# Kernel tuning notes

Hardware: AMD Instinct MI355X
Metric: run time of the kernel (lower is better)

Reference implementation:

```python
import jax, jax.numpy as jnp
import numpy as np

B, S, D, H = 2, 2048, 1024, 16
DH = D // H  # dim_per_head = 64


def setup_inputs() -> dict:
    key = jax.random.key(0)
    ks = jax.random.split(key, 12)
    scale = 1.0 / np.sqrt(D)
    inp = {
        "key": jax.random.normal(ks[0], (B, S, D), jnp.float32),
        "value": jax.random.normal(ks[1], (B, S, D), jnp.float32),
        "query": jax.random.normal(ks[2], (B, S, D), jnp.float32),
        "mask": jax.random.randint(ks[3], (B, S, S), 0, 2) == 1,
        "Wq": jax.random.normal(ks[4], (D, D), jnp.float32) * scale,
        "bq": jnp.zeros((D,), jnp.float32),
        "Wk": jax.random.normal(ks[5], (D, D), jnp.float32) * scale,
        "bk": jnp.zeros((D,), jnp.float32),
        "Wv": jax.random.normal(ks[6], (D, D), jnp.float32) * scale,
        "bv": jnp.zeros((D,), jnp.float32),
        "Wo": jax.random.normal(ks[7], (D, D), jnp.float32) * scale,
        "bo": jnp.zeros((D,), jnp.float32),
    }
    return inp


def reference(key, value, query, mask, Wq, bq, Wk, bk, Wv, bv, Wo, bo):
    b, s, d = query.shape
    dh = d // H

    def split_heads(x):  # [b, s, d] -> [b, H, s, dh]
        return x.reshape(b, -1, H, dh).transpose(0, 2, 1, 3)

    q = split_heads(query @ Wq + bq) / jnp.sqrt(jnp.float32(dh))
    k = split_heads(key @ Wk + bk)
    v = split_heads(value @ Wv + bv)

    scores = jnp.einsum("bhqd,bhkd->bhqk", q, k)  # [b, H, s, s]
    scores = jnp.where(mask[:, None, :, :], jnp.float32(-1e18), scores)
    attn = jax.nn.softmax(scores, axis=-1)  # dropout is identity in eval
    ctx = jnp.einsum("bhqk,bhkd->bhqd", attn, v)
    ctx = ctx.transpose(0, 2, 1, 3).reshape(b, s, d)
    return ctx @ Wo + bo
```

## Files before the change

kernel.cpp:

```cpp
#include <hip/hip_runtime.h>
#include <hip/hip_bf16.h>

#define BATCH  2
#define SEQ    2048
#define DMODEL 1024
#define NHEAD  16
#define DHEAD  64
#define NTOK   (BATCH * SEQ)

using f32x4 = __attribute__((ext_vector_type(4))) float;
using s16x4 = __attribute__((ext_vector_type(4))) short;
using s16x8 = __attribute__((ext_vector_type(8))) short;

__device__ __forceinline__ short f2bf(float f) {
  __hip_bfloat16 h = __float2bfloat16(f);
  return *(short*)&h;
}

__device__ __forceinline__ void gload_lds16(const short* g, short* l) {
  __builtin_amdgcn_global_load_lds(
      (const __attribute__((address_space(1))) void*)g,
      (__attribute__((address_space(3))) void*)l, 16, 0, 0);
}

__global__ __launch_bounds__(256) void wtrans_kernel(
    const float* __restrict__ Wq, const float* __restrict__ Wk,
    const float* __restrict__ Wv, const float* __restrict__ Wo,
    short* __restrict__ Wt) {
  __shared__ short tile[64][72];
  const float* W = blockIdx.z == 0 ? Wq : blockIdx.z == 1 ? Wk
                 : blockIdx.z == 2 ? Wv : Wo;
  short* out = Wt + (size_t)blockIdx.z * DMODEL * DMODEL;
  int k0 = blockIdx.x * 64, n0 = blockIdx.y * 64;
  int t = threadIdx.x;
#pragma unroll
  for (int i = 0; i < 4; ++i) {
    int idx = t + i * 256;
    int row = idx >> 4, c4 = idx & 15;
    f32x4 v = *(const f32x4*)(W + (size_t)(k0 + row) * DMODEL + n0 + c4 * 4);
    s16x4 p;
    p[0] = f2bf(v[0]); p[1] = f2bf(v[1]); p[2] = f2bf(v[2]); p[3] = f2bf(v[3]);
    *(s16x4*)&tile[row][c4 * 4] = p;
  }
  __syncthreads();
#pragma unroll
  for (int i = 0; i < 2; ++i) {
    int idx = t + i * 256;
    int nrow = idx >> 3, c8 = idx & 7;
    s16x8 p;
#pragma unroll
    for (int j = 0; j < 8; ++j) p[j] = tile[c8 * 8 + j][nrow];
    *(s16x8*)(out + (size_t)(n0 + nrow) * DMODEL + k0 + c8 * 8) = p;
  }
}

__global__ __launch_bounds__(256) void mpack_kernel(
    const int* __restrict__ mask, unsigned long long* __restrict__ Mp) {
  const int total_words = BATCH * SEQ * (SEQ / 64);
  int lane = threadIdx.x & 63;
  int wv = blockIdx.x * 4 + (threadIdx.x >> 6);
  int nw = gridDim.x * 4;
  for (int w = wv; w < total_words; w += nw) {
    int mv = mask[(size_t)w * 64 + lane];
    unsigned long long bits = __ballot(mv != 0);
    if (lane == 0) Mp[w] = bits;
  }
}

__global__ __launch_bounds__(256) void proj_qkv_kernel(
    const float* __restrict__ Xq, const float* __restrict__ Xk,
    const float* __restrict__ Xv, const short* __restrict__ Wt,
    const float* __restrict__ bq, const float* __restrict__ bk,
    const float* __restrict__ bv, short* __restrict__ QKV) {
  __shared__ short As[128][32];
  __shared__ short Bs[128][32];
  const int sel = blockIdx.z;
  const float* X    = sel == 0 ? Xq : sel == 1 ? Xk : Xv;
  const float* bias = sel == 0 ? bq : sel == 1 ? bk : bv;
  const short* Wsel = Wt + (size_t)sel * DMODEL * DMODEL;
  short* Obuf = QKV + (size_t)sel * ((size_t)BATCH * NHEAD * SEQ * DHEAD);
  const float scale = sel == 0 ? 0.18033688011111793f : 1.0f;

  int m0 = blockIdx.x * 128, n0 = blockIdx.y * 128;
  int t = threadIdx.x, wid = t >> 6, lane = t & 63;
  int lr = lane & 15, lg = lane >> 4;
  int wr = wid >> 1, wc = wid & 1;
  f32x4 acc[4][4] = {};

  for (int kt = 0; kt < DMODEL / 32; ++kt) {
    int k0 = kt * 32;
    __syncthreads();
#pragma unroll
    for (int i = 0; i < 2; ++i) {
      int c = i * 256 + t;
      short* lbase = &Bs[0][0] + (size_t)((i * 256 + (t & ~63)) << 3);
      gload_lds16(Wsel + (size_t)(n0 + (c >> 2)) * DMODEL + k0 + ((c & 3) << 3),
                  lbase);
    }
#pragma unroll
    for (int i = 0; i < 2; ++i) {
      int idx = t + i * 256, row = idx >> 2, c8 = idx & 3;
      const float* src = X + (size_t)(m0 + row) * DMODEL + k0 + c8 * 8;
      f32x4 v0 = *(const f32x4*)src;
      f32x4 v1 = *(const f32x4*)(src + 4);
      s16x8 p;
      p[0] = f2bf(v0[0]); p[1] = f2bf(v0[1]); p[2] = f2bf(v0[2]); p[3] = f2bf(v0[3]);
      p[4] = f2bf(v1[0]); p[5] = f2bf(v1[1]); p[6] = f2bf(v1[2]); p[7] = f2bf(v1[3]);
      *(s16x8*)&As[row][c8 * 8] = p;
    }
    __syncthreads();
    s16x8 afr[4], bfr[4];
#pragma unroll
    for (int mi = 0; mi < 4; ++mi)
      afr[mi] = *(const s16x8*)&As[wr * 64 + mi * 16 + lr][lg * 8];
#pragma unroll
    for (int ni = 0; ni < 4; ++ni)
      bfr[ni] = *(const s16x8*)&Bs[wc * 64 + ni * 16 + lr][lg * 8];
#pragma unroll
    for (int mi = 0; mi < 4; ++mi)
#pragma unroll
      for (int ni = 0; ni < 4; ++ni)
        acc[mi][ni] = __builtin_amdgcn_mfma_f32_16x16x32_bf16(
            afr[mi], bfr[ni], acc[mi][ni], 0, 0, 0);
  }
#pragma unroll
  for (int mi = 0; mi < 4; ++mi)
#pragma unroll
    for (int ni = 0; ni < 4; ++ni) {
      int n = n0 + wc * 64 + ni * 16 + lr;
      float bv_ = bias[n];
      int h = n >> 6, d = n & 63;
#pragma unroll
      for (int r = 0; r < 4; ++r) {
        int m = m0 + wr * 64 + mi * 16 + lg * 4 + r;
        int b = m >> 11, s = m & (SEQ - 1);
        float val = (acc[mi][ni][r] + bv_) * scale;
        Obuf[((size_t)(b * NHEAD + h) * SEQ + s) * DHEAD + d] = f2bf(val);
      }
    }
}

__global__ __launch_bounds__(256) void attn_kernel(
    const short* __restrict__ Qb, const short* __restrict__ Kb,
    const short* __restrict__ Vb, const unsigned long long* __restrict__ Mp,
    short* __restrict__ Ctx) {
  __shared__ short Ks[64 * 64];
  __shared__ short Vt[64 * 64];
  __shared__ short Ps[4 * 16 * 64];
  int qt = blockIdx.x, bh = blockIdx.y;
  int b = bh >> 4, h = bh & 15;
  int q0 = qt * 64;
  int t = threadIdx.x, wid = t >> 6, lane = t & 63;
  int lr = lane & 15, lg = lane >> 4;
  int lr7 = lr & 7;

  const short* Qrow = Qb + ((size_t)bh * SEQ + q0 + wid * 16 + lr) * DHEAD;
  s16x8 qf[2];
  qf[0] = *(const s16x8*)(Qrow + lg * 8);
  qf[1] = *(const s16x8*)(Qrow + 32 + lg * 8);

  const short* KbBase = Kb + (size_t)bh * SEQ * DHEAD;
  const short* VbBase = Vb + (size_t)bh * SEQ * DHEAD;

  float m_run = -1e30f, l_run = 0.f;
  f32x4 o_acc[4] = {};

  const unsigned long long* mrow =
      Mp + ((size_t)b * SEQ + q0 + wid * 16 + lr) * (SEQ / 64);
  unsigned long long mw = mrow[0];

  s16x8 kreg[2], vreg[2];
#pragma unroll
  for (int i = 0; i < 2; ++i) {
    kreg[i] = *(const s16x8*)(KbBase + (size_t)((t >> 3) + i * 32) * DHEAD + (t & 7) * 8);
    vreg[i] = *(const s16x8*)(VbBase + (size_t)lane * DHEAD + (wid + i * 4) * 8);
  }

  for (int kt = 0; kt < SEQ / 64; ++kt) {
    unsigned long long mw_cur = mw;
    __syncthreads();
#pragma unroll
    for (int i = 0; i < 2; ++i) {
      int krow = (t >> 3) + i * 32, kc = t & 7;
      *(s16x8*)&Ks[krow * 64 + ((kc ^ (krow & 7)) << 3)] = kreg[i];
      int vc8 = wid + i * 4;
#pragma unroll
      for (int j = 0; j < 8; ++j) {
        int d = vc8 * 8 + j;
        Vt[d * 64 + ((((lane >> 3) ^ (d & 7)) << 3) | (lane & 7))] = vreg[i][j];
      }
    }
    __syncthreads();
    if (kt + 1 < SEQ / 64) {
      int k0n = (kt + 1) * 64;
#pragma unroll
      for (int i = 0; i < 2; ++i) {
        kreg[i] = *(const s16x8*)(KbBase + (size_t)(k0n + (t >> 3) + i * 32) * DHEAD + (t & 7) * 8);
        vreg[i] = *(const s16x8*)(VbBase + (size_t)(k0n + lane) * DHEAD + (wid + i * 4) * 8);
      }
      mw = mrow[kt + 1];
    }

    f32x4 sfr[4];
    __builtin_amdgcn_s_setprio(1);
#pragma unroll
    for (int nf = 0; nf < 4; ++nf) {
      int row = nf * 16 + lr;
      s16x8 kf0 = *(const s16x8*)&Ks[row * 64 + ((lg ^ lr7) << 3)];
      s16x8 kf1 = *(const s16x8*)&Ks[row * 64 + (((4 + lg) ^ lr7) << 3)];
      f32x4 c = {};
      c = __builtin_amdgcn_mfma_f32_16x16x32_bf16(kf0, qf[0], c, 0, 0, 0);
      c = __builtin_amdgcn_mfma_f32_16x16x32_bf16(kf1, qf[1], c, 0, 0, 0);
      sfr[nf] = c;
    }
    __builtin_amdgcn_s_setprio(0);

    unsigned w0 = (unsigned)(mw_cur >> (lg * 4));
    unsigned w1 = (unsigned)(mw_cur >> (lg * 4 + 32));
#pragma unroll
    for (int nf = 0; nf < 4; ++nf)
#pragma unroll
      for (int r = 0; r < 4; ++r) {
        unsigned bit = (nf < 2) ? (w0 >> (nf * 16 + r)) : (w1 >> ((nf - 2) * 16 + r));
        if (bit & 1u) sfr[nf][r] = -1e30f;
      }
    float tm = fmaxf(fmaxf(fmaxf(sfr[0][0], sfr[0][1]), fmaxf(sfr[0][2], sfr[0][3])),
                     fmaxf(fmaxf(sfr[1][0], sfr[1][1]), fmaxf(sfr[1][2], sfr[1][3])));
    float tm2 = fmaxf(fmaxf(fmaxf(sfr[2][0], sfr[2][1]), fmaxf(sfr[2][2], sfr[2][3])),
                      fmaxf(fmaxf(sfr[3][0], sfr[3][1]), fmaxf(sfr[3][2], sfr[3][3])));
    tm = fmaxf(tm, tm2);
    tm = fmaxf(tm, __shfl_xor(tm, 16, 64));
    tm = fmaxf(tm, __shfl_xor(tm, 32, 64));

    bool small = __all(tm <= m_run + 8.0f);
    if (!small) {
      float mnew = fmaxf(m_run, tm);
      float scl = __builtin_amdgcn_exp2f(m_run - mnew);
      m_run = mnew;
      l_run *= scl;
      float scl_o[4];
#pragma unroll
      for (int r = 0; r < 4; ++r) scl_o[r] = __shfl(scl, lg * 4 + r, 64);
#pragma unroll
      for (int nf = 0; nf < 4; ++nf)
#pragma unroll
        for (int r = 0; r < 4; ++r) o_acc[nf][r] *= scl_o[r];
    }
    float ps4[4];
#pragma unroll
    for (int nf = 0; nf < 4; ++nf) {
#pragma unroll
      for (int r = 0; r < 4; ++r)
        sfr[nf][r] = __builtin_amdgcn_exp2f(sfr[nf][r] - m_run);
      ps4[nf] = (sfr[nf][0] + sfr[nf][1]) + (sfr[nf][2] + sfr[nf][3]);
    }
    float ps = (ps4[0] + ps4[1]) + (ps4[2] + ps4[3]);
    ps += __shfl_xor(ps, 16, 64);
    ps += __shfl_xor(ps, 32, 64);
    l_run += ps;

    int psbase = wid * (16 * 64) + lr * 64;
#pragma unroll
    for (int nf = 0; nf < 4; ++nf) {
      s16x4 pk;
#pragma unroll
      for (int r = 0; r < 4; ++r) pk[r] = f2bf(sfr[nf][r]);
      *(s16x4*)&Ps[psbase + ((((2 * nf + (lg >> 1)) ^ lr7) << 3) | ((lg & 1) << 2))] = pk;
    }
    asm volatile("s_waitcnt lgkmcnt(0)" ::: "memory");
    __builtin_amdgcn_sched_barrier(0);

    __builtin_amdgcn_s_setprio(1);
#pragma unroll
    for (int ks = 0; ks < 2; ++ks) {
      s16x8 pf = *(const s16x8*)&Ps[psbase + (((ks * 4 + lg) ^ lr7) << 3)];
#pragma unroll
      for (int nf = 0; nf < 4; ++nf) {
        int d = nf * 16 + lr;
        s16x8 vf = *(const s16x8*)&Vt[d * 64 + (((ks * 4 + lg) ^ lr7) << 3)];
        o_acc[nf] = __builtin_amdgcn_mfma_f32_16x16x32_bf16(pf, vf, o_acc[nf], 0, 0, 0);
      }
    }
    __builtin_amdgcn_s_setprio(0);
  }
  float l_o[4];
#pragma unroll
  for (int r = 0; r < 4; ++r) l_o[r] = __shfl(l_run, lg * 4 + r, 64);
#pragma unroll
  for (int nf = 0; nf < 4; ++nf)
#pragma unroll
    for (int r = 0; r < 4; ++r) {
      int srow = q0 + wid * 16 + lg * 4 + r;
      float val = o_acc[nf][r] / l_o[r];
      Ctx[((size_t)b * SEQ + srow) * DMODEL + h * DHEAD + nf * 16 + lr] = f2bf(val);
    }
}

__global__ __launch_bounds__(256) void proj_out_kernel(
    const short* __restrict__ Ctx, const short* __restrict__ Wot,
    const float* __restrict__ bo, float* __restrict__ Out) {
  __shared__ short As[128][32];
  __shared__ short Bs[128][32];
  int m0 = blockIdx.x * 128, n0 = blockIdx.y * 128;
  int t = threadIdx.x, wid = t >> 6, lane = t & 63;
  int lr = lane & 15, lg = lane >> 4;
  int wr = wid >> 1, wc = wid & 1;
  f32x4 acc[4][4] = {};

  for (int kt = 0; kt < DMODEL / 32; ++kt) {
    int k0 = kt * 32;
    __syncthreads();
#pragma unroll
    for (int i = 0; i < 2; ++i) {
      int c = i * 256 + t;
      size_t lofs = (size_t)((i * 256 + (t & ~63)) << 3);
      gload_lds16(Ctx + (size_t)(m0 + (c >> 2)) * DMODEL + k0 + ((c & 3) << 3),
                  &As[0][0] + lofs);
      gload_lds16(Wot + (size_t)(n0 + (c >> 2)) * DMODEL + k0 + ((c & 3) << 3),
                  &Bs[0][0] + lofs);
    }
    __syncthreads();
    s16x8 afr[4], bfr[4];
#pragma unroll
    for (int mi = 0; mi < 4; ++mi)
      afr[mi] = *(const s16x8*)&As[wr * 64 + mi * 16 + lr][lg * 8];
#pragma unroll
    for (int ni = 0; ni < 4; ++ni)
      bfr[ni] = *(const s16x8*)&Bs[wc * 64 + ni * 16 + lr][lg * 8];
#pragma unroll
    for (int mi = 0; mi < 4; ++mi)
#pragma unroll
      for (int ni = 0; ni < 4; ++ni)
        acc[mi][ni] = __builtin_amdgcn_mfma_f32_16x16x32_bf16(
            afr[mi], bfr[ni], acc[mi][ni], 0, 0, 0);
  }
#pragma unroll
  for (int mi = 0; mi < 4; ++mi)
#pragma unroll
    for (int ni = 0; ni < 4; ++ni) {
      int n = n0 + wc * 64 + ni * 16 + lr;
      float bv_ = bo[n];
#pragma unroll
      for (int r = 0; r < 4; ++r) {
        int m = m0 + wr * 64 + mi * 16 + lg * 4 + r;
        Out[(size_t)m * DMODEL + n] = acc[mi][ni][r] + bv_;
      }
    }
}

extern "C" void kernel_launch(void* const* d_in, const int* in_sizes, int n_in,
                              void* d_out, int out_size, void* d_ws, size_t ws_size,
                              hipStream_t stream) {
  const float* key_in   = (const float*)d_in[0];
  const float* value_in = (const float*)d_in[1];
  const float* query_in = (const float*)d_in[2];
  const int*   mask     = (const int*)d_in[3];
  const float* Wq = (const float*)d_in[4];
  const float* bq = (const float*)d_in[5];
  const float* Wk = (const float*)d_in[6];
  const float* bk = (const float*)d_in[7];
  const float* Wv = (const float*)d_in[8];
  const float* bv = (const float*)d_in[9];
  const float* Wo = (const float*)d_in[10];
  const float* bo = (const float*)d_in[11];
  float* out = (float*)d_out;

  short* ws = (short*)d_ws;
  const size_t WSZ   = (size_t)DMODEL * DMODEL;
  const size_t QKVSZ = (size_t)BATCH * NHEAD * SEQ * DHEAD;
  short* Wt  = ws;
  short* QKV = ws + 4 * WSZ;
  short* Qb  = QKV;
  short* Kb  = QKV + QKVSZ;
  short* Vb  = QKV + 2 * QKVSZ;
  short* Ctx = QKV + 3 * QKVSZ;
  unsigned long long* Mp = (unsigned long long*)ws;

  wtrans_kernel<<<dim3(16, 16, 4), 256, 0, stream>>>(Wq, Wk, Wv, Wo, Wt);
  proj_qkv_kernel<<<dim3(32, 8, 3), 256, 0, stream>>>(
      query_in, key_in, value_in, Wt, bq, bk, bv, QKV);
  mpack_kernel<<<dim3(1024), 256, 0, stream>>>(mask, Mp);
  attn_kernel<<<dim3(32, 32), 256, 0, stream>>>(Qb, Kb, Vb, Mp, Ctx);
  proj_out_kernel<<<dim3(32, 8), 256, 0, stream>>>(Ctx, Wt + 3 * WSZ, bo, out);
}
```

Measured before the change: 195.7 us.

## Store V transposed from projection and double-buffer K/V via direct global-to-LDS loads

The QKV projection now writes V in a per-head transposed [dh, seq] layout with packed 4-element stores. This lets the attention kernel fetch both K and V tiles with global_load_lds directly into pre-swizzled LDS, removing the register staging and the scalar element-wise transpose into LDS. K/V LDS buffers are doubled so the next tile loads while the current one is computed, leaving one barrier per iteration. The cost is twice the LDS for K/V, which may reduce occupancy, and a wait on vmcnt(0) at the end of each iteration.

```diff
diff --git a/kernel.cpp b/kernel.cpp
--- a/kernel.cpp
+++ b/kernel.cpp
@@ -123,29 +123,47 @@
         acc[mi][ni] = __builtin_amdgcn_mfma_f32_16x16x32_bf16(
             afr[mi], bfr[ni], acc[mi][ni], 0, 0, 0);
   }
-#pragma unroll
-  for (int mi = 0; mi < 4; ++mi)
-#pragma unroll
-    for (int ni = 0; ni < 4; ++ni) {
-      int n = n0 + wc * 64 + ni * 16 + lr;
-      float bv_ = bias[n];
-      int h = n >> 6, d = n & 63;
-#pragma unroll
-      for (int r = 0; r < 4; ++r) {
-        int m = m0 + wr * 64 + mi * 16 + lg * 4 + r;
-        int b = m >> 11, s = m & (SEQ - 1);
-        float val = (acc[mi][ni][r] + bv_) * scale;
-        Obuf[((size_t)(b * NHEAD + h) * SEQ + s) * DHEAD + d] = f2bf(val);
+  if (sel == 2) {
+    int bq_ = m0 >> 11;
+    int s0 = (m0 & (SEQ - 1)) + wr * 64 + lg * 4;
+#pragma unroll
+    for (int mi = 0; mi < 4; ++mi)
+#pragma unroll
+      for (int ni = 0; ni < 4; ++ni) {
+        int n = n0 + wc * 64 + ni * 16 + lr;
+        float bv_ = bias[n];
+        int h = n >> 6, d = n & 63;
+        s16x4 pk;
+#pragma unroll
+        for (int r = 0; r < 4; ++r) pk[r] = f2bf(acc[mi][ni][r] + bv_);
+        *(s16x4*)&Obuf[((size_t)(bq_ * NHEAD + h) * DHEAD + d) * SEQ
+                       + s0 + mi * 16] = pk;
       }
-    }
+  } else {
+#pragma unroll
+    for (int mi = 0; mi < 4; ++mi)
+#pragma unroll
+      for (int ni = 0; ni < 4; ++ni) {
+        int n = n0 + wc * 64 + ni * 16 + lr;
+        float bv_ = bias[n];
+        int h = n >> 6, d = n & 63;
+#pragma unroll
+        for (int r = 0; r < 4; ++r) {
+          int m = m0 + wr * 64 + mi * 16 + lg * 4 + r;
+          int b = m >> 11, s = m & (SEQ - 1);
+          float val = (acc[mi][ni][r] + bv_) * scale;
+          Obuf[((size_t)(b * NHEAD + h) * SEQ + s) * DHEAD + d] = f2bf(val);
+        }
+      }
+  }
 }
 
 __global__ __launch_bounds__(256) void attn_kernel(
     const short* __restrict__ Qb, const short* __restrict__ Kb,
-    const short* __restrict__ Vb, const unsigned long long* __restrict__ Mp,
+    const short* __restrict__ VbT, const unsigned long long* __restrict__ Mp,
     short* __restrict__ Ctx) {
-  __shared__ short Ks[64 * 64];
-  __shared__ short Vt[64 * 64];
+  __shared__ short Ks[2][64 * 64];
+  __shared__ short Vt[2][64 * 64];
   __shared__ short Ps[4 * 16 * 64];
   int qt = blockIdx.x, bh = blockIdx.y;
   int b = bh >> 4, h = bh & 15;
@@ -159,55 +177,52 @@
   qf[0] = *(const s16x8*)(Qrow + lg * 8);
   qf[1] = *(const s16x8*)(Qrow + 32 + lg * 8);
 
-  const short* KbBase = Kb + (size_t)bh * SEQ * DHEAD;
-  const short* VbBase = Vb + (size_t)bh * SEQ * DHEAD;
+  const short* KbB = Kb + (size_t)bh * SEQ * DHEAD;
+  const short* VtB = VbT + (size_t)bh * DHEAD * SEQ;
+
+  const int srow = lane >> 3;
+  const int schunk = ((lane & 7) ^ srow) * 8;
 
   float m_run = -1e30f, l_run = 0.f;
   f32x4 o_acc[4] = {};
 
   const unsigned long long* mrow =
       Mp + ((size_t)b * SEQ + q0 + wid * 16 + lr) * (SEQ / 64);
-  unsigned long long mw = mrow[0];
-
-  s16x8 kreg[2], vreg[2];
-#pragma unroll
-  for (int i = 0; i < 2; ++i) {
-    kreg[i] = *(const s16x8*)(KbBase + (size_t)((t >> 3) + i * 32) * DHEAD + (t & 7) * 8);
-    vreg[i] = *(const s16x8*)(VbBase + (size_t)lane * DHEAD + (wid + i * 4) * 8);
-  }
-
+
+#define STAGE(bufi, k0s)                                                      \
+  {                                                                           \
+    _Pragma("unroll")                                                         \
+    for (int i = 0; i < 2; ++i) {                                             \
+      int rbase = wid * 16 + i * 8;                                           \
+      gload_lds16(KbB + (size_t)((k0s) + rbase + srow) * DHEAD + schunk,      \
+                  &Ks[bufi][rbase * 64]);                                     \
+      gload_lds16(VtB + (size_t)(rbase + srow) * SEQ + (k0s) + schunk,        \
+                  &Vt[bufi][rbase * 64]);                                     \
+    }                                                                         \
+  }
+
+  unsigned long long mw_cur = mrow[0];
+  STAGE(0, 0);
+  asm volatile("s_waitcnt vmcnt(0)" ::: "memory");
+  __syncthreads();
+
+  int cur = 0;
   for (int kt = 0; kt < SEQ / 64; ++kt) {
-    unsigned long long mw_cur = mw;
-    __syncthreads();
-#pragma unroll
-    for (int i = 0; i < 2; ++i) {
-      int krow = (t >> 3) + i * 32, kc = t & 7;
-      *(s16x8*)&Ks[krow * 64 + ((kc ^ (krow & 7)) << 3)] = kreg[i];
-      int vc8 = wid + i * 4;
-#pragma unroll
-      for (int j = 0; j < 8; ++j) {
-        int d = vc8 * 8 + j;
-        Vt[d * 64 + ((((lane >> 3) ^ (d & 7)) << 3) | (lane & 7))] = vreg[i][j];
-      }
-    }
-    __syncthreads();
+    unsigned long long mw_next = 0;
     if (kt + 1 < SEQ / 64) {
-      int k0n = (kt + 1) * 64;
-#pragma unroll
-      for (int i = 0; i < 2; ++i) {
-        kreg[i] = *(const s16x8*)(KbBase + (size_t)(k0n + (t >> 3) + i * 32) * DHEAD + (t & 7) * 8);
-        vreg[i] = *(const s16x8*)(VbBase + (size_t)(k0n + lane) * DHEAD + (wid + i * 4) * 8);
-      }
-      mw = mrow[kt + 1];
-    }
+      STAGE(cur ^ 1, (kt + 1) * 64);
+      mw_next = mrow[kt + 1];
+    }
+    const short* KsC = Ks[cur];
+    const short* VtC = Vt[cur];
 
     f32x4 sfr[4];
     __builtin_amdgcn_s_setprio(1);
 #pragma unroll
     for (int nf = 0; nf < 4; ++nf) {
       int row = nf * 16 + lr;
-      s16x8 kf0 = *(const s16x8*)&Ks[row * 64 + ((lg ^ lr7) << 3)];
-      s16x8 kf1 = *(const s16x8*)&Ks[row * 64 + (((4 + lg) ^ lr7) << 3)];
+      s16x8 kf0 = *(const s16x8*)&KsC[row * 64 + ((lg ^ lr7) << 3)];
+      s16x8 kf1 = *(const s16x8*)&KsC[row * 64 + (((4 + lg) ^ lr7) << 3)];
       f32x4 c = {};
       c = __builtin_amdgcn_mfma_f32_16x16x32_bf16(kf0, qf[0], c, 0, 0, 0);
       c = __builtin_amdgcn_mfma_f32_16x16x32_bf16(kf1, qf[1], c, 0, 0, 0);
@@ -277,12 +292,18 @@
 #pragma unroll
       for (int nf = 0; nf < 4; ++nf) {
         int d = nf * 16 + lr;
-        s16x8 vf = *(const s16x8*)&Vt[d * 64 + (((ks * 4 + lg) ^ lr7) << 3)];
+        s16x8 vf = *(const s16x8*)&VtC[d * 64 + (((ks * 4 + lg) ^ lr7) << 3)];
         o_acc[nf] = __builtin_amdgcn_mfma_f32_16x16x32_bf16(pf, vf, o_acc[nf], 0, 0, 0);
       }
     }
     __builtin_amdgcn_s_setprio(0);
-  }
+
+    asm volatile("s_waitcnt vmcnt(0)" ::: "memory");
+    __syncthreads();
+    cur ^= 1;
+    mw_cur = mw_next;
+  }
+#undef STAGE
   float l_o[4];
 #pragma unroll
   for (int r = 0; r < 4; ++r) l_o[r] = __shfl(l_run, lg * 4 + r, 64);
@@ -290,9 +311,9 @@
   for (int nf = 0; nf < 4; ++nf)
 #pragma unroll
     for (int r = 0; r < 4; ++r) {
-      int srow = q0 + wid * 16 + lg * 4 + r;
+      int srow_ = q0 + wid * 16 + lg * 4 + r;
       float val = o_acc[nf][r] / l_o[r];
-      Ctx[((size_t)b * SEQ + srow) * DMODEL + h * DHEAD + nf * 16 + lr] = f2bf(val);
+      Ctx[((size_t)b * SEQ + srow_) * DMODEL + h * DHEAD + nf * 16 + lr] = f2bf(val);
     }
 }
 
@@ -372,7 +393,7 @@
   short* QKV = ws + 4 * WSZ;
   short* Qb  = QKV;
   short* Kb  = QKV + QKVSZ;
-  short* Vb  = QKV + 2 * QKVSZ;
+  short* VbT = QKV + 2 * QKVSZ;
   short* Ctx = QKV + 3 * QKVSZ;
   unsigned long long* Mp = (unsigned long long*)ws;
 
@@ -380,6 +401,6 @@
   proj_qkv_kernel<<<dim3(32, 8, 3), 256, 0, stream>>>(
       query_in, key_in, value_in, Wt, bq, bk, bv, QKV);
   mpack_kernel<<<dim3(1024), 256, 0, stream>>>(mask, Mp);
-  attn_kernel<<<dim3(32, 32), 256, 0, stream>>>(Qb, Kb, Vb, Mp, Ctx);
+  attn_kernel<<<dim3(32, 32), 256, 0, stream>>>(Qb, Kb, VbT, Mp, Ctx);
   proj_out_kernel<<<dim3(32, 8), 256, 0, stream>>>(Ctx, Wt + 3 * WSZ, bo, out);
 }
```

New measurement: 185.1 us. 5.4% less time.
